# Kernel optimization log

Hardware: AMD Instinct MI355X
Metric: run time of the kernel (lower is better)

## Reference

```python
import jax, jax.numpy as jnp
import numpy as np

B, IN, H, D, C, K = 4096, 128, 256, 32, 8, 256
HS = D // 2  # structure_filter hidden (latent_dim > 2)
EPS = 1e-6
MAX_NORM = 0.99


def _gelu(t):
    return jax.nn.gelu(t, approximate=False)  # torch nn.GELU default = exact erf


def _project_to_ball(z):
    norm = jnp.maximum(jnp.linalg.norm(z, axis=-1, keepdims=True), EPS)
    scale = jnp.minimum(MAX_NORM / norm, 1.0)
    return z * scale


def _hyperbolic_distance(xp, yp):
    # Poincare-ball distance: arccosh(1 + 2*|x-y|^2 / ((1-|x|^2)(1-|y|^2)))
    sq = jnp.sum((xp - yp) ** 2, axis=-1)
    xn = jnp.sum(xp * xp, axis=-1)
    yn = jnp.sum(yp * yp, axis=-1)
    denom = jnp.maximum((1.0 - xn) * (1.0 - yn), EPS)
    arg = jnp.maximum(1.0 + 2.0 * sq / denom, 1.0 + EPS)
    return jnp.arccosh(arg)


def setup_inputs() -> dict:
    key = jax.random.key(0)
    ks = jax.random.split(key, 14)
    n = lambda k, shape, s: (jax.random.normal(k, shape, dtype=jnp.float32) * s)
    centers = jax.random.normal(ks[7], (C, D), dtype=jnp.float32)
    centers = centers / jnp.maximum(jnp.linalg.norm(centers, axis=-1, keepdims=True), EPS)
    return {
        "x": jax.random.normal(ks[0], (B, IN), dtype=jnp.float32),
        "W1": n(ks[1], (IN, H), 0.05), "b1": jnp.zeros((H,), jnp.float32),
        "W2": n(ks[2], (H, H), 0.05), "b2": jnp.zeros((H,), jnp.float32),
        "Wv": n(ks[3], (H, D), 0.05), "bv": jnp.zeros((D,), jnp.float32),
        "centers": centers,
        "codebook": n(ks[8], (C, K, D), 0.02),
        "Ws1": n(ks[9], (D, HS), 0.1), "bs1": jnp.zeros((HS,), jnp.float32),
        "Ws2": n(ks[10], (HS, D), 0.1), "bs2": jnp.zeros((D,), jnp.float32),
    }


def reference(x, W1, b1, W2, b2, Wv, bv, centers, codebook, Ws1, bs1, Ws2, bs2):
    sg = jax.lax.stop_gradient
    feats = _gelu(_gelu(x @ W1 + b1) @ W2 + b2)          # [B,H]
    v = feats @ Wv + bv                                   # [B,D]
    scores = (v @ centers.T) / jnp.sqrt(jnp.asarray(D, v.dtype))
    router = jax.nn.softmax(scores, axis=-1)              # [B,C]
    K_chart = jnp.argmax(router, axis=1)                  # [B]
    c_bar = router @ centers                              # [B,D]
    v_local = v - c_bar                                   # [B,D]
    diff = v_local[:, None, None, :] - codebook[None]     # [B,C,K,D]
    dist = jnp.sum(diff * diff, axis=-1)                  # [B,C,K]
    indices = jnp.argmin(dist, axis=-1)                   # [B,C]
    z_q_all = codebook[jnp.arange(C)[None, :], indices]   # [B,C,D]
    v_bc = jnp.broadcast_to(v_local[:, None, :], z_q_all.shape)
    v_proj = _project_to_ball(v_bc)
    w_det = sg(router)
    d_cb = _hyperbolic_distance(z_q_all, sg(v_proj))      # [B,C]
    codebook_loss = jnp.sum(jnp.mean(d_cb ** 2 * w_det, axis=0))
    d_cm = _hyperbolic_distance(sg(z_q_all), v_proj)
    commitment = jnp.sum(jnp.mean(d_cm ** 2 * w_det, axis=0))
    vq_loss = codebook_loss + 0.25 * commitment
    z_q_blended = jnp.sum(z_q_all * router[..., None], axis=1)  # [B,D]
    K_code = jnp.take_along_axis(indices, K_chart[:, None], axis=1)[:, 0]
    delta = v_local[:, None, :] - sg(z_q_all)             # [B,C,D]
    z_n_all = _gelu(delta @ Ws1 + bs1) @ Ws2 + bs2        # [B,C,D]
    z_n = jnp.sum(z_n_all * router[..., None], axis=1)    # [B,D]
    z_tex = (v_local - sg(z_q_blended)) - z_n
    z_q_st = v_local + sg(z_q_blended - v_local)
    z_geo = c_bar + z_q_st + z_n
    return (K_chart, K_code, z_n, z_tex, router, z_geo, vq_loss, indices, z_n_all, c_bar, v_local)
```

## Files before the change

kernel.cpp:

```cpp
#include <hip/hip_runtime.h>
#include <math.h>

#define NB 4096
#define NIN 128
#define NH 256
#define ND 32
#define NC 8
#define NK 256
#define NHS 16

#define OFF_KCHART 0
#define OFF_KCODE  4096
#define OFF_ZN     8192
#define OFF_ZTEX   (OFF_ZN + 4096*32)
#define OFF_ROUTER (OFF_ZTEX + 4096*32)
#define OFF_ZGEO   (OFF_ROUTER + 4096*8)
#define OFF_LOSS   (OFF_ZGEO + 4096*32)
#define OFF_IND    (OFF_LOSS + 1)
#define OFF_ZNALL  (OFF_IND + 4096*8)
#define OFF_CBAR   (OFF_ZNALL + 4096*8*32)
#define OFF_VLOC   (OFF_CBAR + 4096*32)

__device__ __forceinline__ float gelu_exact(float x) {
    return x * (erff(x / 1.41421356237309504f) + 1.0f) * 0.5f;
}

template<int K>
__global__ __launch_bounds__(256)
void gemm_bias_gelu(const float* __restrict__ A, const float* __restrict__ W,
                    const float* __restrict__ bias, float* __restrict__ out) {
    const int N = 256;
    __shared__ float sB[2][32][68];
    const int t  = threadIdx.x;
    const int n0 = blockIdx.x * 64;
    const int r0 = blockIdx.y * 32;
    const int ty = t >> 4, tx = t & 15;
    const int bk = t >> 4, bc = t & 15;

    float4 bias4 = *(const float4*)(bias + n0 + tx * 4);

    float4 pb0 = *(const float4*)(W + bk * N + n0 + bc * 4);
    float4 pb1 = *(const float4*)(W + (bk + 16) * N + n0 + bc * 4);

    const float* Ab0 = A + (r0 + ty * 2 + 0) * K;
    const float* Ab1 = A + (r0 + ty * 2 + 1) * K;
    float ac[2][4], an[2][4];
    {
        float4 c0 = *(const float4*)(Ab0 + 0), c1 = *(const float4*)(Ab1 + 0);
        ac[0][0]=c0.x; ac[0][1]=c0.y; ac[0][2]=c0.z; ac[0][3]=c0.w;
        ac[1][0]=c1.x; ac[1][1]=c1.y; ac[1][2]=c1.z; ac[1][3]=c1.w;
        float4 d0 = *(const float4*)(Ab0 + 4), d1 = *(const float4*)(Ab1 + 4);
        an[0][0]=d0.x; an[0][1]=d0.y; an[0][2]=d0.z; an[0][3]=d0.w;
        an[1][0]=d1.x; an[1][1]=d1.y; an[1][2]=d1.z; an[1][3]=d1.w;
    }

    float acc[2][4];
    #pragma unroll
    for (int i = 0; i < 2; i++)
        #pragma unroll
        for (int j = 0; j < 4; j++) acc[i][j] = 0.f;

    int buf = 0;
    for (int kk = 0; kk < K; kk += 32) {
        *(float4*)(&sB[buf][bk][bc*4])    = pb0;
        *(float4*)(&sB[buf][bk+16][bc*4]) = pb1;
        __syncthreads();
        if (kk + 32 < K) {
            pb0 = *(const float4*)(W + (kk + 32 + bk) * N + n0 + bc * 4);
            pb1 = *(const float4*)(W + (kk + 32 + bk + 16) * N + n0 + bc * 4);
        }
        #pragma unroll
        for (int c = 0; c < 8; c++) {
            int knext = kk + (c + 2) * 4;
            if (knext > K - 4) knext = K - 4;
            float4 p0 = *(const float4*)(Ab0 + knext);
            float4 p1 = *(const float4*)(Ab1 + knext);
            #pragma unroll
            for (int u = 0; u < 4; u++) {
                float4 bv = *(const float4*)(&sB[buf][c * 4 + u][tx * 4]);
                float bb[4] = {bv.x, bv.y, bv.z, bv.w};
                #pragma unroll
                for (int j = 0; j < 4; j++) {
                    acc[0][j] = fmaf(ac[0][u], bb[j], acc[0][j]);
                    acc[1][j] = fmaf(ac[1][u], bb[j], acc[1][j]);
                }
            }
            #pragma unroll
            for (int u = 0; u < 4; u++) { ac[0][u] = an[0][u]; ac[1][u] = an[1][u]; }
            an[0][0]=p0.x; an[0][1]=p0.y; an[0][2]=p0.z; an[0][3]=p0.w;
            an[1][0]=p1.x; an[1][1]=p1.y; an[1][2]=p1.z; an[1][3]=p1.w;
        }
        buf ^= 1;
    }
    float bb4[4] = {bias4.x, bias4.y, bias4.z, bias4.w};
    #pragma unroll
    for (int i = 0; i < 2; i++) {
        int row = r0 + ty * 2 + i;
        float4 o;
        float* op = (float*)&o;
        #pragma unroll
        for (int j = 0; j < 4; j++) op[j] = gelu_exact(acc[i][j] + bb4[j]);
        *(float4*)(out + row * N + n0 + tx * 4) = o;
    }
}

__global__ __launch_bounds__(256)
void router_kernel(const float* __restrict__ feats, const float* __restrict__ Wv,
                   const float* __restrict__ bv, const float* __restrict__ centers,
                   float* __restrict__ out, float* __restrict__ vloc_ws) {
    __shared__ float sWvT[ND][260];
    __shared__ float sCent[NC * ND];
    __shared__ float sV[8][ND + 2];
    __shared__ float sScore[8][NC];
    __shared__ float sRout[8][NC];
    const int t = threadIdx.x;
    const int row0 = blockIdx.x * 8;
    {
        #pragma unroll
        for (int q = 0; q < 8; q++) {
            int id = t + q * 256;
            int k = id >> 3, c4 = (id & 7) * 4;
            float4 w = ((const float4*)Wv)[id];
            sWvT[c4 + 0][k] = w.x;
            sWvT[c4 + 1][k] = w.y;
            sWvT[c4 + 2][k] = w.z;
            sWvT[c4 + 3][k] = w.w;
        }
        if (t < 64) ((float4*)sCent)[t] = ((const float4*)centers)[t];
    }
    __syncthreads();
    const int r = t >> 5, cp = t & 31;
    const int row = row0 + r;
    float a0 = bv[cp];
    const float4* f4 = (const float4*)(feats + row * NH);
    for (int k4 = 0; k4 < NH / 4; k4++) {
        float4 f = f4[k4];
        float4 w = *(const float4*)(&sWvT[cp][k4 * 4]);
        a0 = fmaf(f.x, w.x, a0);
        a0 = fmaf(f.y, w.y, a0);
        a0 = fmaf(f.z, w.z, a0);
        a0 = fmaf(f.w, w.w, a0);
    }
    sV[r][cp] = a0;
    __syncthreads();
    if (t < 64) {
        int rr = t >> 3, c = t & 7;
        float s = 0.f;
        #pragma unroll
        for (int k = 0; k < ND; k++) s = fmaf(sV[rr][k], sCent[c * ND + k], s);
        sScore[rr][c] = s / 5.65685424949238f;
    }
    __syncthreads();
    if (t < 8) {
        const int rr = t, grow = row0 + rr;
        float sc[NC];
        float m = -3.4e38f; int kmax = 0;
        #pragma unroll
        for (int c = 0; c < NC; c++) {
            float s = sScore[rr][c];
            sc[c] = s;
            if (s > m) { m = s; kmax = c; }
        }
        float ssum = 0.f;
        #pragma unroll
        for (int c = 0; c < NC; c++) { float e = expf(sc[c] - m); sc[c] = e; ssum += e; }
        float inv = 1.f / ssum;
        #pragma unroll
        for (int c = 0; c < NC; c++) {
            float rv = sc[c] * inv;
            sRout[rr][c] = rv;
            out[OFF_ROUTER + grow * NC + c] = rv;
        }
        out[OFF_KCHART + grow] = (float)kmax;
    }
    __syncthreads();
    {
        const int col = cp;
        float cb = 0.f;
        #pragma unroll
        for (int c = 0; c < NC; c++) cb = fmaf(sRout[r][c], sCent[c * ND + col], cb);
        float vl = sV[r][col] - cb;
        out[OFF_CBAR + row * ND + col] = cb;
        out[OFF_VLOC + row * ND + col] = vl;
        vloc_ws[row * ND + col] = vl;
    }
}

__global__ __launch_bounds__(256)
void vq_chart(const float* __restrict__ codebook, const float* __restrict__ vloc_ws,
              const float* __restrict__ Ws1, const float* __restrict__ bs1,
              const float* __restrict__ Ws2, const float* __restrict__ bs2,
              float* __restrict__ out, float* __restrict__ loss_partial) {
    __shared__ float sCB[NK][36];
    __shared__ float sEn2[NK];
    __shared__ float sV[64][36];
    __shared__ float sBest[8][64];
    __shared__ int   sBidx[8][64];
    __shared__ int   sSel[64];
    __shared__ float sRoutv[64];
    __shared__ float sPscale[64];
    __shared__ float sLossArr[64];
    __shared__ float sWs1[ND][17];
    __shared__ float sWs2[NHS][33];
    __shared__ float sbs1[NHS], sbs2v[ND];
    const int t = threadIdx.x;
    const int c = blockIdx.x & 7;
    const int row0 = (blockIdx.x >> 3) * 64;

    {
        const float4* src = (const float4*)(codebook + c * NK * ND);
        #pragma unroll
        for (int q = 0; q < 8; q++) {
            int id = t + q * 256;
            int code = id >> 3, kq = (id & 7) * 4;
            *(float4*)(&sCB[code][kq]) = src[id];
        }
        #pragma unroll
        for (int q = 0; q < 2; q++) {
            int id = t + q * 256;
            int rr = id >> 3, kq = (id & 7) * 4;
            *(float4*)(&sV[rr][kq]) = ((const float4*)(vloc_ws + row0 * ND))[id];
        }
    }
    if (t < 128) {
        float4 w = ((const float4*)Ws1)[t];
        int k = t >> 2, o = (t & 3) * 4;
        sWs1[k][o] = w.x; sWs1[k][o+1] = w.y; sWs1[k][o+2] = w.z; sWs1[k][o+3] = w.w;
    } else {
        int u = t - 128;
        float4 w = ((const float4*)Ws2)[u];
        int k = u >> 3, o = (u & 7) * 4;
        sWs2[k][o] = w.x; sWs2[k][o+1] = w.y; sWs2[k][o+2] = w.z; sWs2[k][o+3] = w.w;
    }
    if (t < NHS) sbs1[t] = bs1[t];
    else if (t < NHS + ND) sbs2v[t - NHS] = bs2[t - NHS];
    if (t < 64) sRoutv[t] = out[OFF_ROUTER + (row0 + t) * NC + c];
    __syncthreads();
    {
        float s = 0.f;
        #pragma unroll
        for (int q = 0; q < 8; q++) {
            float4 e = *(const float4*)(&sCB[t][q * 4]);
            s = fmaf(e.x, e.x, s); s = fmaf(e.y, e.y, s);
            s = fmaf(e.z, e.z, s); s = fmaf(e.w, e.w, s);
        }
        sEn2[t] = s;
    }
    __syncthreads();

    const int r = t & 31, g = t >> 5;
    float vl0[ND], vl1[ND];
    #pragma unroll
    for (int q = 0; q < 8; q++) {
        float4 a = *(const float4*)(&sV[r][q * 4]);
        vl0[q*4] = a.x; vl0[q*4+1] = a.y; vl0[q*4+2] = a.z; vl0[q*4+3] = a.w;
        float4 b = *(const float4*)(&sV[r + 32][q * 4]);
        vl1[q*4] = b.x; vl1[q*4+1] = b.y; vl1[q*4+2] = b.z; vl1[q*4+3] = b.w;
    }
    float best0 = 3.4e38f, best1 = 3.4e38f;
    int bi0 = 0, bi1 = 0;
    for (int j = 0; j < 32; j++) {
        const int code = g * 32 + j;
        float dot0 = 0.f, dot1 = 0.f;
        #pragma unroll
        for (int q = 0; q < 8; q++) {
            float4 e = *(const float4*)(&sCB[code][q * 4]);
            dot0 = fmaf(vl0[q*4+0], e.x, dot0); dot1 = fmaf(vl1[q*4+0], e.x, dot1);
            dot0 = fmaf(vl0[q*4+1], e.y, dot0); dot1 = fmaf(vl1[q*4+1], e.y, dot1);
            dot0 = fmaf(vl0[q*4+2], e.z, dot0); dot1 = fmaf(vl1[q*4+2], e.z, dot1);
            dot0 = fmaf(vl0[q*4+3], e.w, dot0); dot1 = fmaf(vl1[q*4+3], e.w, dot1);
        }
        const float en2 = sEn2[code];
        float d0 = en2 - 2.f * dot0;
        float d1 = en2 - 2.f * dot1;
        if (d0 < best0) { best0 = d0; bi0 = code; }
        if (d1 < best1) { best1 = d1; bi1 = code; }
    }
    sBest[g][r] = best0;      sBidx[g][r] = bi0;
    sBest[g][r + 32] = best1; sBidx[g][r + 32] = bi1;
    __syncthreads();
    if (t < 64) {
        float bb = sBest[0][t]; int ii = sBidx[0][t];
        #pragma unroll
        for (int gg = 1; gg < 8; gg++) {
            float v = sBest[gg][t];
            if (v < bb) { bb = v; ii = sBidx[gg][t]; }
        }
        sSel[t] = ii;
        out[OFF_IND + (row0 + t) * NC + c] = (float)ii;
        float vn2 = 0.f;
        #pragma unroll
        for (int k = 0; k < ND; k++) { float v = sV[t][k]; vn2 = fmaf(v, v, vn2); }
        float norm = fmaxf(sqrtf(vn2), 1e-6f);
        sPscale[t] = fminf(0.99f / norm, 1.0f);
    }
    __syncthreads();

    const int i = t & 15, r16 = t >> 4;
    const float b1r = sbs1[i];
    const float bo0 = sbs2v[2*i], bo1 = sbs2v[2*i+1];
    #pragma unroll
    for (int pass = 0; pass < 4; pass++) {
        const int lrow = pass * 16 + r16;
        const int grow = row0 + lrow;
        const int sel = sSel[lrow];
        const float rc = sRoutv[lrow];
        const float ps = sPscale[lrow];
        float acc1 = b1r;
        #pragma unroll
        for (int k = 0; k < ND; k++) {
            float dlt = sV[lrow][k] - sCB[sel][k];
            acc1 = fmaf(dlt, sWs1[k][i], acc1);
        }
        float h = gelu_exact(acc1);
        float a0 = bo0, a1 = bo1;
        #pragma unroll
        for (int k = 0; k < NHS; k++) {
            float s1k = __shfl(h, k, 16);
            a0 = fmaf(s1k, sWs2[k][2*i],   a0);
            a1 = fmaf(s1k, sWs2[k][2*i+1], a1);
        }
        out[OFF_ZNALL + (grow * NC + c) * ND + 2*i]     = a0;
        out[OFF_ZNALL + (grow * NC + c) * ND + 2*i + 1] = a1;
        const float e0 = sCB[sel][2*i], e1 = sCB[sel][2*i+1];
        float yp0 = sV[lrow][2*i] * ps, yp1 = sV[lrow][2*i+1] * ps;
        float d0 = e0 - yp0, d1 = e1 - yp1;
        float sq = fmaf(d0, d0, d1 * d1);
        float xn = fmaf(e0, e0, e1 * e1);
        float yn = fmaf(yp0, yp0, yp1 * yp1);
        #pragma unroll
        for (int m = 1; m < 16; m <<= 1) {
            sq += __shfl_xor(sq, m, 16);
            xn += __shfl_xor(xn, m, 16);
            yn += __shfl_xor(yn, m, 16);
        }
        if (i == 0) {
            float denom = fmaxf((1.f - xn) * (1.f - yn), 1e-6f);
            float arg = fmaxf(1.f + 2.f * sq / denom, 1.f + 1e-6f);
            float dd = acoshf(arg);
            sLossArr[lrow] = dd * dd * rc;
        }
    }
    __syncthreads();
    if (t < 64) {
        float v = sLossArr[t];
        #pragma unroll
        for (int off = 32; off > 0; off >>= 1) v += __shfl_down(v, off, 64);
        if (t == 0) loss_partial[blockIdx.x] = v;
    }
}

__global__ __launch_bounds__(256)
void finalize2_kernel(const float* __restrict__ codebook, const float* __restrict__ vloc_ws,
                      float* __restrict__ out, const float* __restrict__ partials) {
    const int gid = blockIdx.x * 256 + threadIdx.x;
    const int row = gid >> 5;
    const int col = gid & 31;
    float rout[NC]; int ind[NC];
    #pragma unroll
    for (int cc = 0; cc < NC; cc++) {
        rout[cc] = out[OFF_ROUTER + row * NC + cc];
        ind[cc]  = (int)out[OFF_IND + row * NC + cc];
    }
    float zn = 0.f, zq = 0.f;
    #pragma unroll
    for (int cc = 0; cc < NC; cc++) {
        const float rcc = rout[cc];
        zn = fmaf(out[OFF_ZNALL + (row * NC + cc) * ND + col], rcc, zn);
        zq = fmaf(codebook[(cc * NK + ind[cc]) * ND + col], rcc, zq);
    }
    const float vl = vloc_ws[row * ND + col];
    const float cb = out[OFF_CBAR + row * ND + col];
    out[OFF_ZN   + row * ND + col] = zn;
    out[OFF_ZTEX + row * ND + col] = vl - zq - zn;
    out[OFF_ZGEO + row * ND + col] = cb + zq + zn;
    if (col == 0) {
        int kc = (int)out[OFF_KCHART + row];
        out[OFF_KCODE + row] = out[OFF_IND + row * NC + kc];
    }
    if (blockIdx.x == 0) {
        __shared__ float sTmp[4];
        const int t = threadIdx.x;
        float v = partials[t] + partials[t + 256];
        #pragma unroll
        for (int off = 32; off > 0; off >>= 1) v += __shfl_down(v, off, 64);
        if ((t & 63) == 0) sTmp[t >> 6] = v;
        __syncthreads();
        if (t == 0) out[OFF_LOSS] = 1.25f * (sTmp[0] + sTmp[1] + sTmp[2] + sTmp[3]) / 4096.f;
    }
}

extern "C" void kernel_launch(void* const* d_in, const int* in_sizes, int n_in,
                              void* d_out, int out_size, void* d_ws, size_t ws_size,
                              hipStream_t stream) {
    const float* x        = (const float*)d_in[0];
    const float* W1       = (const float*)d_in[1];
    const float* b1       = (const float*)d_in[2];
    const float* W2       = (const float*)d_in[3];
    const float* b2       = (const float*)d_in[4];
    const float* Wv       = (const float*)d_in[5];
    const float* bv       = (const float*)d_in[6];
    const float* centers  = (const float*)d_in[7];
    const float* codebook = (const float*)d_in[8];
    const float* Ws1      = (const float*)d_in[9];
    const float* bs1      = (const float*)d_in[10];
    const float* Ws2      = (const float*)d_in[11];
    const float* bs2      = (const float*)d_in[12];
    float* out = (float*)d_out;
    float* ws  = (float*)d_ws;

    float* h1       = ws;
    float* feats    = ws + 4096 * 256;
    float* vloc     = ws + 2 * 4096 * 256;
    float* partials = ws + 2 * 4096 * 256 + 4096 * 32;

    gemm_bias_gelu<128><<<dim3(4, 128), dim3(256), 0, stream>>>(x, W1, b1, h1);
    gemm_bias_gelu<256><<<dim3(4, 128), dim3(256), 0, stream>>>(h1, W2, b2, feats);
    router_kernel<<<dim3(512), dim3(256), 0, stream>>>(feats, Wv, bv, centers, out, vloc);
    vq_chart<<<dim3(512), dim3(256), 0, stream>>>(codebook, vloc, Ws1, bs1, Ws2, bs2, out, partials);
    finalize2_kernel<<<dim3(512), dim3(256), 0, stream>>>(codebook, vloc, out, partials);
}
```

Measured before the change: 59.96 us.

## Fuse five kernels into one persistent kernel with atomic grid barriers

Merges the two GEMMs, router, VQ and finalize kernels into a single 512-block launch whose phases are separated by a software grid barrier on an atomic counter, with shared memory overlaid through a union. The aim is to remove four kernel launch gaps and the tail drain between dependent kernels. It also XOR-swizzles the transposed Wv tile in shared memory to cut bank conflicts. The barrier needs all 512 blocks to be co-resident (launch_bounds 256,2 plus the large union footprint) or the kernel deadlocks, and it adds a memset plus spin-wait cost at each phase.

```diff
diff --git a/kernel.cpp b/kernel.cpp
--- a/kernel.cpp
+++ b/kernel.cpp
@@ -25,15 +25,37 @@
     return x * (erff(x / 1.41421356237309504f) + 1.0f) * 0.5f;
 }
 
+__device__ __forceinline__ void gbar(int* bar, int target) {
+    __syncthreads();
+    if (threadIdx.x == 0) {
+        __threadfence();
+        __hip_atomic_fetch_add(bar, 1, __ATOMIC_ACQ_REL, __HIP_MEMORY_SCOPE_AGENT);
+        while (__hip_atomic_load(bar, __ATOMIC_ACQUIRE, __HIP_MEMORY_SCOPE_AGENT) < target) {
+            __builtin_amdgcn_s_sleep(1);
+        }
+    }
+    __syncthreads();
+}
+
+struct SmemGemm   { float sB[2][32][68]; };
+struct SmemRouter { float sWv[32 * 272]; float sCent[NC * ND];
+                    float sV[8][ND + 2]; float sScore[8][NC];
+                    float sRout[8][NC]; };
+struct SmemVq     { float sCB[NK][36]; float sEn2[NK]; float sV[64][36];
+                    float sBest[8][64]; int sBidx[8][64]; int sSel[64];
+                    float sRoutv[64]; float sPscale[64]; float sLossArr[64];
+                    float sWs1[ND][17]; float sWs2[NHS][33];
+                    float sbs1[NHS]; float sbs2v[ND]; };
+union SmemAll { SmemGemm g; SmemRouter r; SmemVq v; float sTmp[4]; };
+
 template<int K>
-__global__ __launch_bounds__(256)
-void gemm_bias_gelu(const float* __restrict__ A, const float* __restrict__ W,
-                    const float* __restrict__ bias, float* __restrict__ out) {
+__device__ __forceinline__
+void gemm_phase(const float* __restrict__ A, const float* __restrict__ W,
+                const float* __restrict__ bias, float* __restrict__ outp,
+                SmemGemm& sm, int b, int t) {
     const int N = 256;
-    __shared__ float sB[2][32][68];
-    const int t  = threadIdx.x;
-    const int n0 = blockIdx.x * 64;
-    const int r0 = blockIdx.y * 32;
+    const int n0 = (b & 3) * 64;
+    const int r0 = (b >> 2) * 32;
     const int ty = t >> 4, tx = t & 15;
     const int bk = t >> 4, bc = t & 15;
 
@@ -62,8 +84,8 @@
 
     int buf = 0;
     for (int kk = 0; kk < K; kk += 32) {
-        *(float4*)(&sB[buf][bk][bc*4])    = pb0;
-        *(float4*)(&sB[buf][bk+16][bc*4]) = pb1;
+        *(float4*)(&sm.sB[buf][bk][bc*4])    = pb0;
+        *(float4*)(&sm.sB[buf][bk+16][bc*4]) = pb1;
         __syncthreads();
         if (kk + 32 < K) {
             pb0 = *(const float4*)(W + (kk + 32 + bk) * N + n0 + bc * 4);
@@ -77,7 +99,7 @@
             float4 p1 = *(const float4*)(Ab1 + knext);
             #pragma unroll
             for (int u = 0; u < 4; u++) {
-                float4 bv = *(const float4*)(&sB[buf][c * 4 + u][tx * 4]);
+                float4 bv = *(const float4*)(&sm.sB[buf][c * 4 + u][tx * 4]);
                 float bb[4] = {bv.x, bv.y, bv.z, bv.w};
                 #pragma unroll
                 for (int j = 0; j < 4; j++) {
@@ -100,55 +122,52 @@
         float* op = (float*)&o;
         #pragma unroll
         for (int j = 0; j < 4; j++) op[j] = gelu_exact(acc[i][j] + bb4[j]);
-        *(float4*)(out + row * N + n0 + tx * 4) = o;
-    }
-}
-
-__global__ __launch_bounds__(256)
-void router_kernel(const float* __restrict__ feats, const float* __restrict__ Wv,
-                   const float* __restrict__ bv, const float* __restrict__ centers,
-                   float* __restrict__ out, float* __restrict__ vloc_ws) {
-    __shared__ float sWvT[ND][260];
-    __shared__ float sCent[NC * ND];
-    __shared__ float sV[8][ND + 2];
-    __shared__ float sScore[8][NC];
-    __shared__ float sRout[8][NC];
-    const int t = threadIdx.x;
-    const int row0 = blockIdx.x * 8;
+        *(float4*)(outp + row * N + n0 + tx * 4) = o;
+    }
+}
+
+__device__ __forceinline__
+void router_phase(const float* __restrict__ feats, const float* __restrict__ Wv,
+                  const float* __restrict__ bv, const float* __restrict__ centers,
+                  float* __restrict__ out, float* __restrict__ vloc_ws,
+                  SmemRouter& sm, int b, int t) {
+    const int row0 = b * 8;
     {
         #pragma unroll
         for (int q = 0; q < 8; q++) {
             int id = t + q * 256;
             int k = id >> 3, c4 = (id & 7) * 4;
+            int kb = k >> 2, kr = k & 3;
             float4 w = ((const float4*)Wv)[id];
-            sWvT[c4 + 0][k] = w.x;
-            sWvT[c4 + 1][k] = w.y;
-            sWvT[c4 + 2][k] = w.z;
-            sWvT[c4 + 3][k] = w.w;
-        }
-        if (t < 64) ((float4*)sCent)[t] = ((const float4*)centers)[t];
+            sm.sWv[(c4+0) * 272 + ((kb ^ ((c4+0) & 7)) << 2) + kr] = w.x;
+            sm.sWv[(c4+1) * 272 + ((kb ^ ((c4+1) & 7)) << 2) + kr] = w.y;
+            sm.sWv[(c4+2) * 272 + ((kb ^ ((c4+2) & 7)) << 2) + kr] = w.z;
+            sm.sWv[(c4+3) * 272 + ((kb ^ ((c4+3) & 7)) << 2) + kr] = w.w;
+        }
+        if (t < 64) ((float4*)sm.sCent)[t] = ((const float4*)centers)[t];
     }
     __syncthreads();
     const int r = t >> 5, cp = t & 31;
     const int row = row0 + r;
+    const int cbase = cp * 272, cxor = cp & 7;
     float a0 = bv[cp];
     const float4* f4 = (const float4*)(feats + row * NH);
     for (int k4 = 0; k4 < NH / 4; k4++) {
         float4 f = f4[k4];
-        float4 w = *(const float4*)(&sWvT[cp][k4 * 4]);
+        float4 w = *(const float4*)(&sm.sWv[cbase + ((k4 ^ cxor) << 2)]);
         a0 = fmaf(f.x, w.x, a0);
         a0 = fmaf(f.y, w.y, a0);
         a0 = fmaf(f.z, w.z, a0);
         a0 = fmaf(f.w, w.w, a0);
     }
-    sV[r][cp] = a0;
+    sm.sV[r][cp] = a0;
     __syncthreads();
     if (t < 64) {
         int rr = t >> 3, c = t & 7;
         float s = 0.f;
         #pragma unroll
-        for (int k = 0; k < ND; k++) s = fmaf(sV[rr][k], sCent[c * ND + k], s);
-        sScore[rr][c] = s / 5.65685424949238f;
+        for (int k = 0; k < ND; k++) s = fmaf(sm.sV[rr][k], sm.sCent[c * ND + k], s);
+        sm.sScore[rr][c] = s / 5.65685424949238f;
     }
     __syncthreads();
     if (t < 8) {
@@ -157,7 +176,7 @@
         float m = -3.4e38f; int kmax = 0;
         #pragma unroll
         for (int c = 0; c < NC; c++) {
-            float s = sScore[rr][c];
+            float s = sm.sScore[rr][c];
             sc[c] = s;
             if (s > m) { m = s; kmax = c; }
         }
@@ -168,7 +187,7 @@
         #pragma unroll
         for (int c = 0; c < NC; c++) {
             float rv = sc[c] * inv;
-            sRout[rr][c] = rv;
+            sm.sRout[rr][c] = rv;
             out[OFF_ROUTER + grow * NC + c] = rv;
         }
         out[OFF_KCHART + grow] = (float)kmax;
@@ -178,34 +197,22 @@
         const int col = cp;
         float cb = 0.f;
         #pragma unroll
-        for (int c = 0; c < NC; c++) cb = fmaf(sRout[r][c], sCent[c * ND + col], cb);
-        float vl = sV[r][col] - cb;
+        for (int c = 0; c < NC; c++) cb = fmaf(sm.sRout[r][c], sm.sCent[c * ND + col], cb);
+        float vl = sm.sV[r][col] - cb;
         out[OFF_CBAR + row * ND + col] = cb;
         out[OFF_VLOC + row * ND + col] = vl;
         vloc_ws[row * ND + col] = vl;
     }
 }
 
-__global__ __launch_bounds__(256)
-void vq_chart(const float* __restrict__ codebook, const float* __restrict__ vloc_ws,
+__device__ __forceinline__
+void vq_phase(const float* __restrict__ codebook, const float* __restrict__ vloc_ws,
               const float* __restrict__ Ws1, const float* __restrict__ bs1,
               const float* __restrict__ Ws2, const float* __restrict__ bs2,
-              float* __restrict__ out, float* __restrict__ loss_partial) {
-    __shared__ float sCB[NK][36];
-    __shared__ float sEn2[NK];
-    __shared__ float sV[64][36];
-    __shared__ float sBest[8][64];
-    __shared__ int   sBidx[8][64];
-    __shared__ int   sSel[64];
-    __shared__ float sRoutv[64];
-    __shared__ float sPscale[64];
-    __shared__ float sLossArr[64];
-    __shared__ float sWs1[ND][17];
-    __shared__ float sWs2[NHS][33];
-    __shared__ float sbs1[NHS], sbs2v[ND];
-    const int t = threadIdx.x;
-    const int c = blockIdx.x & 7;
-    const int row0 = (blockIdx.x >> 3) * 64;
+              float* __restrict__ out, float* __restrict__ loss_partial,
+              SmemVq& sm, int b, int t) {
+    const int c = b & 7;
+    const int row0 = (b >> 3) * 64;
 
     {
         const float4* src = (const float4*)(codebook + c * NK * ND);
@@ -213,38 +220,40 @@
         for (int q = 0; q < 8; q++) {
             int id = t + q * 256;
             int code = id >> 3, kq = (id & 7) * 4;
-            *(float4*)(&sCB[code][kq]) = src[id];
+            *(float4*)(&sm.sCB[code][kq]) = src[id];
         }
         #pragma unroll
         for (int q = 0; q < 2; q++) {
             int id = t + q * 256;
             int rr = id >> 3, kq = (id & 7) * 4;
-            *(float4*)(&sV[rr][kq]) = ((const float4*)(vloc_ws + row0 * ND))[id];
+            *(float4*)(&sm.sV[rr][kq]) = ((const float4*)(vloc_ws + row0 * ND))[id];
         }
     }
     if (t < 128) {
         float4 w = ((const float4*)Ws1)[t];
         int k = t >> 2, o = (t & 3) * 4;
-        sWs1[k][o] = w.x; sWs1[k][o+1] = w.y; sWs1[k][o+2] = w.z; sWs1[k][o+3] = w.w;
+        sm.sWs1[k][o] = w.x; sm.sWs1[k][o+1] = w.y;
+        sm.sWs1[k][o+2] = w.z; sm.sWs1[k][o+3] = w.w;
     } else {
         int u = t - 128;
         float4 w = ((const float4*)Ws2)[u];
         int k = u >> 3, o = (u & 7) * 4;
-        sWs2[k][o] = w.x; sWs2[k][o+1] = w.y; sWs2[k][o+2] = w.z; sWs2[k][o+3] = w.w;
-    }
-    if (t < NHS) sbs1[t] = bs1[t];
-    else if (t < NHS + ND) sbs2v[t - NHS] = bs2[t - NHS];
-    if (t < 64) sRoutv[t] = out[OFF_ROUTER + (row0 + t) * NC + c];
+        sm.sWs2[k][o] = w.x; sm.sWs2[k][o+1] = w.y;
+        sm.sWs2[k][o+2] = w.z; sm.sWs2[k][o+3] = w.w;
+    }
+    if (t < NHS) sm.sbs1[t] = bs1[t];
+    else if (t < NHS + ND) sm.sbs2v[t - NHS] = bs2[t - NHS];
+    if (t < 64) sm.sRoutv[t] = out[OFF_ROUTER + (row0 + t) * NC + c];
     __syncthreads();
     {
         float s = 0.f;
         #pragma unroll
         for (int q = 0; q < 8; q++) {
-            float4 e = *(const float4*)(&sCB[t][q * 4]);
+            float4 e = *(const float4*)(&sm.sCB[t][q * 4]);
             s = fmaf(e.x, e.x, s); s = fmaf(e.y, e.y, s);
             s = fmaf(e.z, e.z, s); s = fmaf(e.w, e.w, s);
         }
-        sEn2[t] = s;
+        sm.sEn2[t] = s;
     }
     __syncthreads();
 
@@ -252,10 +261,10 @@
     float vl0[ND], vl1[ND];
     #pragma unroll
     for (int q = 0; q < 8; q++) {
-        float4 a = *(const float4*)(&sV[r][q * 4]);
+        float4 a = *(const float4*)(&sm.sV[r][q * 4]);
         vl0[q*4] = a.x; vl0[q*4+1] = a.y; vl0[q*4+2] = a.z; vl0[q*4+3] = a.w;
-        float4 b = *(const float4*)(&sV[r + 32][q * 4]);
-        vl1[q*4] = b.x; vl1[q*4+1] = b.y; vl1[q*4+2] = b.z; vl1[q*4+3] = b.w;
+        float4 bb = *(const float4*)(&sm.sV[r + 32][q * 4]);
+        vl1[q*4] = bb.x; vl1[q*4+1] = bb.y; vl1[q*4+2] = bb.z; vl1[q*4+3] = bb.w;
     }
     float best0 = 3.4e38f, best1 = 3.4e38f;
     int bi0 = 0, bi1 = 0;
@@ -264,66 +273,66 @@
         float dot0 = 0.f, dot1 = 0.f;
         #pragma unroll
         for (int q = 0; q < 8; q++) {
-            float4 e = *(const float4*)(&sCB[code][q * 4]);
+            float4 e = *(const float4*)(&sm.sCB[code][q * 4]);
             dot0 = fmaf(vl0[q*4+0], e.x, dot0); dot1 = fmaf(vl1[q*4+0], e.x, dot1);
             dot0 = fmaf(vl0[q*4+1], e.y, dot0); dot1 = fmaf(vl1[q*4+1], e.y, dot1);
             dot0 = fmaf(vl0[q*4+2], e.z, dot0); dot1 = fmaf(vl1[q*4+2], e.z, dot1);
             dot0 = fmaf(vl0[q*4+3], e.w, dot0); dot1 = fmaf(vl1[q*4+3], e.w, dot1);
         }
-        const float en2 = sEn2[code];
+        const float en2 = sm.sEn2[code];
         float d0 = en2 - 2.f * dot0;
         float d1 = en2 - 2.f * dot1;
         if (d0 < best0) { best0 = d0; bi0 = code; }
         if (d1 < best1) { best1 = d1; bi1 = code; }
     }
-    sBest[g][r] = best0;      sBidx[g][r] = bi0;
-    sBest[g][r + 32] = best1; sBidx[g][r + 32] = bi1;
+    sm.sBest[g][r] = best0;      sm.sBidx[g][r] = bi0;
+    sm.sBest[g][r + 32] = best1; sm.sBidx[g][r + 32] = bi1;
     __syncthreads();
     if (t < 64) {
-        float bb = sBest[0][t]; int ii = sBidx[0][t];
+        float bb = sm.sBest[0][t]; int ii = sm.sBidx[0][t];
         #pragma unroll
         for (int gg = 1; gg < 8; gg++) {
-            float v = sBest[gg][t];
-            if (v < bb) { bb = v; ii = sBidx[gg][t]; }
-        }
-        sSel[t] = ii;
+            float v = sm.sBest[gg][t];
+            if (v < bb) { bb = v; ii = sm.sBidx[gg][t]; }
+        }
+        sm.sSel[t] = ii;
         out[OFF_IND + (row0 + t) * NC + c] = (float)ii;
         float vn2 = 0.f;
         #pragma unroll
-        for (int k = 0; k < ND; k++) { float v = sV[t][k]; vn2 = fmaf(v, v, vn2); }
+        for (int k = 0; k < ND; k++) { float v = sm.sV[t][k]; vn2 = fmaf(v, v, vn2); }
         float norm = fmaxf(sqrtf(vn2), 1e-6f);
-        sPscale[t] = fminf(0.99f / norm, 1.0f);
+        sm.sPscale[t] = fminf(0.99f / norm, 1.0f);
     }
     __syncthreads();
 
     const int i = t & 15, r16 = t >> 4;
-    const float b1r = sbs1[i];
-    const float bo0 = sbs2v[2*i], bo1 = sbs2v[2*i+1];
+    const float b1r = sm.sbs1[i];
+    const float bo0 = sm.sbs2v[2*i], bo1 = sm.sbs2v[2*i+1];
     #pragma unroll
     for (int pass = 0; pass < 4; pass++) {
         const int lrow = pass * 16 + r16;
         const int grow = row0 + lrow;
-        const int sel = sSel[lrow];
-        const float rc = sRoutv[lrow];
-        const float ps = sPscale[lrow];
+        const int sel = sm.sSel[lrow];
+        const float rc = sm.sRoutv[lrow];
+        const float ps = sm.sPscale[lrow];
         float acc1 = b1r;
         #pragma unroll
         for (int k = 0; k < ND; k++) {
-            float dlt = sV[lrow][k] - sCB[sel][k];
-            acc1 = fmaf(dlt, sWs1[k][i], acc1);
+            float dlt = sm.sV[lrow][k] - sm.sCB[sel][k];
+            acc1 = fmaf(dlt, sm.sWs1[k][i], acc1);
         }
         float h = gelu_exact(acc1);
         float a0 = bo0, a1 = bo1;
         #pragma unroll
         for (int k = 0; k < NHS; k++) {
             float s1k = __shfl(h, k, 16);
-            a0 = fmaf(s1k, sWs2[k][2*i],   a0);
-            a1 = fmaf(s1k, sWs2[k][2*i+1], a1);
+            a0 = fmaf(s1k, sm.sWs2[k][2*i],   a0);
+            a1 = fmaf(s1k, sm.sWs2[k][2*i+1], a1);
         }
         out[OFF_ZNALL + (grow * NC + c) * ND + 2*i]     = a0;
         out[OFF_ZNALL + (grow * NC + c) * ND + 2*i + 1] = a1;
-        const float e0 = sCB[sel][2*i], e1 = sCB[sel][2*i+1];
-        float yp0 = sV[lrow][2*i] * ps, yp1 = sV[lrow][2*i+1] * ps;
+        const float e0 = sm.sCB[sel][2*i], e1 = sm.sCB[sel][2*i+1];
+        float yp0 = sm.sV[lrow][2*i] * ps, yp1 = sm.sV[lrow][2*i+1] * ps;
         float d0 = e0 - yp0, d1 = e1 - yp1;
         float sq = fmaf(d0, d0, d1 * d1);
         float xn = fmaf(e0, e0, e1 * e1);
@@ -338,22 +347,23 @@
             float denom = fmaxf((1.f - xn) * (1.f - yn), 1e-6f);
             float arg = fmaxf(1.f + 2.f * sq / denom, 1.f + 1e-6f);
             float dd = acoshf(arg);
-            sLossArr[lrow] = dd * dd * rc;
+            sm.sLossArr[lrow] = dd * dd * rc;
         }
     }
     __syncthreads();
     if (t < 64) {
-        float v = sLossArr[t];
+        float v = sm.sLossArr[t];
         #pragma unroll
         for (int off = 32; off > 0; off >>= 1) v += __shfl_down(v, off, 64);
-        if (t == 0) loss_partial[blockIdx.x] = v;
-    }
-}
-
-__global__ __launch_bounds__(256)
-void finalize2_kernel(const float* __restrict__ codebook, const float* __restrict__ vloc_ws,
-                      float* __restrict__ out, const float* __restrict__ partials) {
-    const int gid = blockIdx.x * 256 + threadIdx.x;
+        if (t == 0) loss_partial[b] = v;
+    }
+}
+
+__device__ __forceinline__
+void finalize_phase(const float* __restrict__ codebook, const float* __restrict__ vloc_ws,
+                    float* __restrict__ out, const float* __restrict__ partials,
+                    float* sTmp, int b, int t) {
+    const int gid = b * 256 + t;
     const int row = gid >> 5;
     const int col = gid & 31;
     float rout[NC]; int ind[NC];
@@ -378,9 +388,7 @@
         int kc = (int)out[OFF_KCHART + row];
         out[OFF_KCODE + row] = out[OFF_IND + row * NC + kc];
     }
-    if (blockIdx.x == 0) {
-        __shared__ float sTmp[4];
-        const int t = threadIdx.x;
+    if (b == 0) {
         float v = partials[t] + partials[t + 256];
         #pragma unroll
         for (int off = 32; off > 0; off >>= 1) v += __shfl_down(v, off, 64);
@@ -388,6 +396,32 @@
         __syncthreads();
         if (t == 0) out[OFF_LOSS] = 1.25f * (sTmp[0] + sTmp[1] + sTmp[2] + sTmp[3]) / 4096.f;
     }
+}
+
+__global__ __launch_bounds__(256, 2)
+void atlas_fused(const float* __restrict__ x, const float* __restrict__ W1,
+                 const float* __restrict__ b1, const float* __restrict__ W2,
+                 const float* __restrict__ b2, const float* __restrict__ Wv,
+                 const float* __restrict__ bv, const float* __restrict__ centers,
+                 const float* __restrict__ codebook, const float* __restrict__ Ws1,
+                 const float* __restrict__ bs1, const float* __restrict__ Ws2,
+                 const float* __restrict__ bs2, float* __restrict__ out,
+                 float* __restrict__ h1, float* __restrict__ feats,
+                 float* __restrict__ vloc, float* __restrict__ partials,
+                 int* __restrict__ bar) {
+    __shared__ SmemAll sm;
+    const int t = threadIdx.x;
+    const int b = blockIdx.x;
+
+    gemm_phase<128>(x, W1, b1, h1, sm.g, b, t);
+    gbar(bar, 512);
+    gemm_phase<256>(h1, W2, b2, feats, sm.g, b, t);
+    gbar(bar, 1024);
+    router_phase(feats, Wv, bv, centers, out, vloc, sm.r, b, t);
+    gbar(bar, 1536);
+    vq_phase(codebook, vloc, Ws1, bs1, Ws2, bs2, out, partials, sm.v, b, t);
+    gbar(bar, 2048);
+    finalize_phase(codebook, vloc, out, partials, sm.sTmp, b, t);
 }
 
 extern "C" void kernel_launch(void* const* d_in, const int* in_sizes, int n_in,
@@ -413,10 +447,10 @@
     float* feats    = ws + 4096 * 256;
     float* vloc     = ws + 2 * 4096 * 256;
     float* partials = ws + 2 * 4096 * 256 + 4096 * 32;
-
-    gemm_bias_gelu<128><<<dim3(4, 128), dim3(256), 0, stream>>>(x, W1, b1, h1);
-    gemm_bias_gelu<256><<<dim3(4, 128), dim3(256), 0, stream>>>(h1, W2, b2, feats);
-    router_kernel<<<dim3(512), dim3(256), 0, stream>>>(feats, Wv, bv, centers, out, vloc);
-    vq_chart<<<dim3(512), dim3(256), 0, stream>>>(codebook, vloc, Ws1, bs1, Ws2, bs2, out, partials);
-    finalize2_kernel<<<dim3(512), dim3(256), 0, stream>>>(codebook, vloc, out, partials);
-}
+    int*   bar      = (int*)(ws + 2 * 4096 * 256 + 4096 * 32 + 1024);
+
+    hipMemsetAsync(bar, 0, 128, stream);
+    atlas_fused<<<dim3(512), dim3(256), 0, stream>>>(
+        x, W1, b1, W2, b2, Wv, bv, centers, codebook,
+        Ws1, bs1, Ws2, bs2, out, h1, feats, vloc, partials, bar);
+}
```

After: 200.5 us. +234.4%, slower.
